# Kernel tuning notes

Hardware: AMD Instinct MI355X
Metric: run time of the kernel (lower is better)

The kernel has to match this reference:

```python
import jax, jax.numpy as jnp
import numpy as np

D, H, W = 128, 96, 96  # voxel grid
EPS = 1e-5

_OFFS = np.array([[dz, dy, dx] for dz in (-1, 0, 1) for dy in (-1, 0, 1) for dx in (-1, 0, 1)], dtype=np.int64)


def _flat(c):
    return (c[:, 0] * H + c[:, 1]) * W + c[:, 2]


def _dilate(coords):
    # union of coords + all 27 offsets, clipped to grid bounds (stride-1, pad-1 SparseConv3d output sites)
    p = coords[None, :, :] + _OFFS[:, None, :]          # [27, N, 3]
    p = p.reshape(-1, 3)
    ok = np.all((p >= 0) & (p < np.array([D, H, W])), axis=1)
    keys = np.unique(_flat(p[ok]))
    out = np.stack([keys // (H * W), (keys // W) % H, keys % W], axis=1)
    return out


def _rulebook(in_coords, out_coords):
    # nb[k, m] = row index into in_coords of (out_coords[m] + off_k), or -1
    lut = -np.ones(D * H * W, dtype=np.int32)
    lut[_flat(in_coords)] = np.arange(len(in_coords), dtype=np.int32)
    nb = np.full((27, len(out_coords)), -1, dtype=np.int32)
    for k, o in enumerate(_OFFS):
        p = out_coords + o
        ok = np.all((p >= 0) & (p < np.array([D, H, W])), axis=1)
        nb[k, ok] = lut[_flat(p[ok])]
    return nb


def setup_inputs() -> dict:
    key = jax.random.key(0)
    ks = jax.random.split(key, 20)
    # active sites: full plane z=64 over 96x96 footprint (surface-like sparse scene)
    yy, xx = np.meshgrid(np.arange(H), np.arange(W), indexing='ij')
    coords0 = np.stack([np.full(H * W, 64), yy.ravel(), xx.ravel()], axis=1).astype(np.int64)
    coords1 = _dilate(coords0)   # 27648 sites
    coords2 = _dilate(coords1)   # 46080 sites
    nb1 = jnp.asarray(_rulebook(coords0, coords1))
    nbs = jnp.asarray(_rulebook(coords1, coords1))
    nb2 = jnp.asarray(_rulebook(coords1, coords2))

    s = 0.05
    inp = {
        'x': jax.random.normal(ks[0], (coords0.shape[0], 256), jnp.float32),
        'w_s1': jax.random.normal(ks[1], (27, 256, 128), jnp.float32) * s,
        'g_s1': jax.random.uniform(ks[2], (128,), jnp.float32, 0.5, 1.5),
        'b_s1': jax.random.normal(ks[3], (128,), jnp.float32) * 0.1,
        'w11': jax.random.normal(ks[4], (27, 128, 128), jnp.float32) * s,
        'g11': jax.random.uniform(ks[5], (128,), jnp.float32, 0.5, 1.5),
        'b11': jax.random.normal(ks[6], (128,), jnp.float32) * 0.1,
        'w12': jax.random.normal(ks[7], (27, 128, 128), jnp.float32) * s,
        'g12': jax.random.uniform(ks[8], (128,), jnp.float32, 0.5, 1.5),
        'b12': jax.random.normal(ks[9], (128,), jnp.float32) * 0.1,
        'w21': jax.random.normal(ks[10], (27, 128, 128), jnp.float32) * s,
        'g21': jax.random.uniform(ks[11], (128,), jnp.float32, 0.5, 1.5),
        'b21': jax.random.normal(ks[12], (128,), jnp.float32) * 0.1,
        'w22': jax.random.normal(ks[13], (27, 128, 128), jnp.float32) * s,
        'g22': jax.random.uniform(ks[14], (128,), jnp.float32, 0.5, 1.5),
        'b22': jax.random.normal(ks[15], (128,), jnp.float32) * 0.1,
        'w_s2': jax.random.normal(ks[16], (27, 128, 32), jnp.float32) * s,
        'g_s2': jax.random.uniform(ks[17], (32,), jnp.float32, 0.5, 1.5),
        'b_s2': jax.random.normal(ks[18], (32,), jnp.float32) * 0.1,
        'nb1': nb1, 'nbs': nbs, 'nb2': nb2,
    }
    return inp


def _sparse_conv(x, nb, w):
    # gather -> GEMM -> accumulate per kernel offset (rulebook semantics of spconv)
    mask = nb >= 0                      # [27, M]
    idx = jnp.where(mask, nb, 0)
    out = jnp.zeros((nb.shape[1], w.shape[2]), x.dtype)
    for k in range(nb.shape[0]):        # fixed 27-offset loop
        g = jnp.where(mask[k][:, None], x[idx[k]], 0.0)  # [M, Cin]
        out = out + g @ w[k]
    return out


def _bn(f, g, b):
    # BatchNorm1d in training mode over active voxel rows (biased variance)
    mu = jnp.mean(f, axis=0)
    var = jnp.mean(jnp.square(f - mu), axis=0)
    return (f - mu) * jax.lax.rsqrt(var + EPS) * g + b


def _block(f, nbs, w1, g1, b1, w2, g2, b2):
    idn = f
    h = jax.nn.relu(_bn(_sparse_conv(f, nbs, w1), g1, b1))
    h = _bn(_sparse_conv(h, nbs, w2), g2, b2)
    return jax.nn.relu(h + idn)


def reference(x, w_s1, g_s1, b_s1, w11, g11, b11, w12, g12, b12,
              w21, g21, b21, w22, g22, b22, w_s2, g_s2, b_s2,
              nb1, nbs, nb2):
    f = jax.nn.relu(_bn(_sparse_conv(x, nb1, w_s1), g_s1, b_s1))          # spconv1
    f = _block(f, nbs, w11, g11, b11, w12, g12, b12)                      # block1 (submanifold)
    f = _block(f, nbs, w21, g21, b21, w22, g22, b22)                      # block2 (submanifold)
    out = jax.nn.relu(_bn(_sparse_conv(f, nb2, w_s2), g_s2, b_s2))        # spconv2
    return out  # features of the final SparseConvTensor, [46080, 32]
```

## Files before the change

kernel.cpp:

```cpp
#include <hip/hip_runtime.h>
#include <stdint.h>

typedef _Float16 f16;
typedef _Float16 f16x8 __attribute__((ext_vector_type(8)));
typedef _Float16 f16x4 __attribute__((ext_vector_type(4)));
typedef float f32x4 __attribute__((ext_vector_type(4)));

#define GAS __attribute__((address_space(1)))
#define LAS __attribute__((address_space(3)))

__device__ __forceinline__ void gl_lds16(const void* g, void* l) {
    __builtin_amdgcn_global_load_lds((const GAS uint32_t*)g, (LAS uint32_t*)l, 16, 0, 0);
}

__global__ __launch_bounds__(256) void zerof(float* __restrict__ p, int n) {
    int i = blockIdx.x * 256 + threadIdx.x;
    if (i < n) p[i] = 0.f;
}

__global__ __launch_bounds__(256) void cvt16(const float* __restrict__ in,
                                             f16* __restrict__ o, long n) {
    long i = (long)blockIdx.x * 256 + threadIdx.x;
    if (i < n) o[i] = (f16)in[i];
}

__global__ __launch_bounds__(256) void wtrans16(const float* __restrict__ w,
                                                f16* __restrict__ wt,
                                                int Cin, int Cout) {
    long i = (long)blockIdx.x * 256 + threadIdx.x;
    long total = 27L * Cin * Cout;
    if (i >= total) return;
    int ci = (int)(i % Cin);
    long t = i / Cin;
    int co = (int)(t % Cout);
    int k  = (int)(t / Cout);
    wt[i] = (f16)w[((long)k * Cin + ci) * Cout + co];
}

template <int LAYER>
__global__ __launch_bounds__(512, 2) void conv_dense(
    const f16* __restrict__ fin, const f16* __restrict__ wt,
    const f16* __restrict__ zrow, float* __restrict__ out,
    float* __restrict__ stats) {
    constexpr int COUT = (LAYER == 2) ? 32 : 128;
    constexpr int INRB = (LAYER == 0) ? 512 : 256;
    constexpr int WRB  = (LAYER == 0) ? 512 : 256;
    constexpr int RT   = (COUT == 128) ? 4 : 2;
    constexpr int CT   = (COUT == 128) ? 4 : 2;
    constexpr int NBCH = COUT / 4;
    extern __shared__ char smem[];
    char* ldsA0 = smem;
    char* ldsA1 = smem + 46080;
    char* ldsB0 = smem + 92160;
    char* ldsB1 = smem + 92160 + COUT * 256;

    const int b = blockIdx.x;
    const int p = b / 72;
    const int t0 = b % 72;
    const int y0 = (t0 / 6) * 8;
    const int x0 = (t0 % 6) * 16;
    const int tid = threadIdx.x;
    const int lane = tid & 63;
    const int wave = tid >> 6;
    const int kh = wave & 1;
    const int pairId = wave >> 1;
    const int q = lane >> 4;
    const int r16 = lane & 15;
    const int wr = ((COUT == 128) ? (pairId >> 1) : pairId) * (RT * 16);
    const int wc = ((COUT == 128) ? (pairId & 1) : 0) * (CT * 16);

    int S = 0;
    int js[3], dzs[3], hs[3];
    if (LAYER == 0) {
        js[0] = 0; dzs[0] = 1 - p; hs[0] = 0;
        js[1] = 0; dzs[1] = 1 - p; hs[1] = 1;
        S = 2;
    } else if (LAYER == 1) {
        for (int dz = -1; dz <= 1; dz++) {
            int j = p + dz;
            if (0 <= j && j < 3) { js[S] = j; dzs[S] = dz; hs[S] = 0; S++; }
        }
    } else {
        for (int dz = -1; dz <= 1; dz++) {
            int j = p + dz - 1;
            if (0 <= j && j < 3) { js[S] = j; dzs[S] = dz; hs[S] = 0; S++; }
        }
    }

    auto stageA = [&](int s, char* buf) {
        const int j = js[s], h = hs[s];
        const long pbase = (long)j * 9216;
        for (int ch = wave; ch < 45; ch += 8) {
            int site = ch * 4 + q;
            int sy = site / 18;
            int sx = site - sy * 18;
            int y = y0 - 1 + sy;
            int x = x0 - 1 + sx;
            int cc = r16 ^ (site & 7);
            bool ok = ((unsigned)y < 96u) & ((unsigned)x < 96u);
            const char* src = ok
                ? (const char*)fin + (pbase + y * 96 + x) * INRB + h * 256 + cc * 16
                : (const char*)zrow + cc * 16;
            gl_lds16(src, buf + ch * 1024);
        }
    };
    auto stageB = [&](int k, int h, char* buf) {
        for (int ch = wave; ch < NBCH; ch += 8) {
            int col = ch * 4 + q;
            int cc = r16 ^ (col & 7);
            const char* src = (const char*)wt + (long)(k * COUT + col) * WRB +
                              h * 256 + cc * 16;
            gl_lds16(src, buf + ch * 1024);
        }
    };

    f32x4 acc[RT][CT];
#pragma unroll
    for (int tr = 0; tr < RT; tr++)
#pragma unroll
        for (int c = 0; c < CT; c++) acc[tr][c] = f32x4{0.f, 0.f, 0.f, 0.f};

    stageA(0, ldsA0);
    stageB((dzs[0] + 1) * 9, hs[0], ldsB0);

    int tap = 0;
    for (int s = 0; s < S; s++) {
        const char* bufA = (s & 1) ? ldsA1 : ldsA0;
#pragma unroll
        for (int i = 0; i < 9; i++, tap++) {
            __syncthreads();
            if (i == 0 && s + 1 < S) stageA(s + 1, ((s + 1) & 1) ? ldsA1 : ldsA0);
            if (tap + 1 < S * 9) {
                int sn = (i == 8) ? s + 1 : s;
                int in2 = (i == 8) ? 0 : i + 1;
                stageB((dzs[sn] + 1) * 9 + in2, hs[sn], ((tap + 1) & 1) ? ldsB1 : ldsB0);
            }
            const char* bufB = (tap & 1) ? ldsB1 : ldsB0;
            const int dy = i / 3 - 1, dx = i % 3 - 1;
#pragma unroll
            for (int kk2 = 0; kk2 < 2; kk2++) {
                const int kk = kh * 2 + kk2;
                f16x8 Af[RT], Bf[CT];
#pragma unroll
                for (int tr = 0; tr < RT; tr++) {
                    int site = (wr / 16 + tr + 1 + dy) * 18 + 1 + dx + r16;
                    Af[tr] = *(const f16x8*)(bufA + site * 256 +
                                             (((kk * 4 + q) ^ (site & 7)) << 4));
                }
#pragma unroll
                for (int c = 0; c < CT; c++) {
                    int col = wc + c * 16 + r16;
                    Bf[c] = *(const f16x8*)(bufB + col * 256 +
                                            (((kk * 4 + q) ^ (col & 7)) << 4));
                }
#pragma unroll
                for (int tr = 0; tr < RT; tr++)
#pragma unroll
                    for (int c = 0; c < CT; c++)
                        acc[tr][c] = __builtin_amdgcn_mfma_f32_16x16x32_f16(
                            Af[tr], Bf[c], acc[tr][c], 0, 0, 0);
            }
        }
    }

    char* xch = smem + 92160;
    constexpr int XR = RT * CT * 1024;
    __syncthreads();
    if (kh == 1) {
#pragma unroll
        for (int tr = 0; tr < RT; tr++)
#pragma unroll
            for (int c = 0; c < CT; c++)
                *(f32x4*)(xch + pairId * XR + (tr * CT + c) * 1024 + lane * 16) =
                    acc[tr][c];
    }
    __syncthreads();
    if (kh == 1) return;
#pragma unroll
    for (int tr = 0; tr < RT; tr++)
#pragma unroll
        for (int c = 0; c < CT; c++)
            acc[tr][c] += *(const f32x4*)(xch + pairId * XR + (tr * CT + c) * 1024 +
                                          lane * 16);

    const long mbase = (long)p * 9216 + (long)y0 * 96 + x0;
#pragma unroll
    for (int c = 0; c < CT; c++) {
        const int col = wc + c * 16 + r16;
        float sum = 0.f, ssq = 0.f;
#pragma unroll
        for (int tr = 0; tr < RT; tr++) {
            const int ly = wr / 16 + tr;
#pragma unroll
            for (int r = 0; r < 4; r++) {
                const int lx = q * 4 + r;
                float v = acc[tr][c][r];
                out[(mbase + ly * 96 + lx) * COUT + col] = v;
                sum += v;
                ssq = fmaf(v, v, ssq);
            }
        }
        sum += __shfl_xor(sum, 16);
        sum += __shfl_xor(sum, 32);
        ssq += __shfl_xor(ssq, 16);
        ssq += __shfl_xor(ssq, 32);
        if (q == 0) {
            atomicAdd(&stats[col], sum);
            atomicAdd(&stats[COUT + col], ssq);
        }
    }
}

__global__ __launch_bounds__(256) void bn_apply4(
    const float4* __restrict__ f, const float* __restrict__ sums,
    const float* __restrict__ g, const float* __restrict__ bta,
    const f16x4* __restrict__ idn, f16* __restrict__ outh,
    float4* __restrict__ outf, long n4, int C, float invM) {
    long i = (long)blockIdx.x * 256 + threadIdx.x;
    if (i >= n4) return;
    int col0 = (int)((i * 4) & (C - 1));
    float4 v = f[i];
    float r[4] = {v.x, v.y, v.z, v.w};
    f16x4 id = {};
    if (idn) id = idn[i];
    f16x4 ho;
#pragma unroll
    for (int j = 0; j < 4; j++) {
        int c = col0 + j;
        float mu = sums[c] * invM;
        float var = sums[C + c] * invM - mu * mu;
        var = fmaxf(var, 0.f);
        float sc = g[c] * rsqrtf(var + 1e-5f);
        float x = (r[j] - mu) * sc + bta[c];
        if (idn) x += (float)id[j];
        x = fmaxf(x, 0.f);
        r[j] = x;
        ho[j] = (f16)x;
    }
    if (outf) outf[i] = make_float4(r[0], r[1], r[2], r[3]);
    else *(f16x4*)(outh + i * 4) = ho;
}

extern "C" void kernel_launch(void* const* d_in, const int* in_sizes, int n_in,
                              void* d_out, int out_size, void* d_ws, size_t ws_size,
                              hipStream_t stream) {
    (void)n_in; (void)out_size; (void)ws_size;
    const float* x    = (const float*)d_in[0];
    const float* w_s1 = (const float*)d_in[1];
    const float* g_s1 = (const float*)d_in[2];
    const float* b_s1 = (const float*)d_in[3];
    const float* w11  = (const float*)d_in[4];
    const float* g11  = (const float*)d_in[5];
    const float* b11  = (const float*)d_in[6];
    const float* w12  = (const float*)d_in[7];
    const float* g12  = (const float*)d_in[8];
    const float* b12  = (const float*)d_in[9];
    const float* w21  = (const float*)d_in[10];
    const float* g21  = (const float*)d_in[11];
    const float* b21  = (const float*)d_in[12];
    const float* w22  = (const float*)d_in[13];
    const float* g22  = (const float*)d_in[14];
    const float* b22  = (const float*)d_in[15];
    const float* w_s2 = (const float*)d_in[16];
    const float* g_s2 = (const float*)d_in[17];
    const float* b_s2 = (const float*)d_in[18];

    const int N0 = in_sizes[0] / 256;
    const int M1 = in_sizes[19] / 27;
    const int M2 = in_sizes[21] / 27;

    char* base = (char*)d_ws;
    size_t off = 0;
    auto alloc = [&](size_t bytes) -> char* {
        off = (off + 255) & ~(size_t)255;
        char* p = base + off;
        off += bytes;
        return p;
    };
    f16* xh  = (f16*)alloc((size_t)N0 * 256 * 2);
    f16* w1  = (f16*)alloc(27UL * 128 * 256 * 2);
    f16* wa1 = (f16*)alloc(27UL * 128 * 128 * 2);
    f16* wa2 = (f16*)alloc(27UL * 128 * 128 * 2);
    f16* wb1 = (f16*)alloc(27UL * 128 * 128 * 2);
    f16* wb2 = (f16*)alloc(27UL * 128 * 128 * 2);
    f16* w2  = (f16*)alloc(27UL * 32 * 128 * 2);
    f16* fA  = (f16*)alloc((size_t)M1 * 128 * 2);
    f16* fB  = (f16*)alloc((size_t)M1 * 128 * 2);
    float* cbuf  = (float*)alloc((size_t)M1 * 128 * 4);
    float* stats = (float*)alloc(1344UL * 4);
    f16*   zrow  = (f16*)alloc(512);

    const int lds01 = 92160 + 2 * 128 * 256;
    const int lds2  = 92160 + 2 * 32 * 256;
    (void)hipFuncSetAttribute((const void*)conv_dense<0>,
                              hipFuncAttributeMaxDynamicSharedMemorySize, lds01);
    (void)hipFuncSetAttribute((const void*)conv_dense<1>,
                              hipFuncAttributeMaxDynamicSharedMemorySize, lds01);
    (void)hipFuncSetAttribute((const void*)conv_dense<2>,
                              hipFuncAttributeMaxDynamicSharedMemorySize, lds2);

    zerof<<<6, 256, 0, stream>>>(stats, 1472);

    long nx = (long)N0 * 256;
    cvt16<<<(int)((nx + 255) / 256), 256, 0, stream>>>(x, xh, nx);
    wtrans16<<<(27 * 256 * 128 + 255) / 256, 256, 0, stream>>>(w_s1, w1, 256, 128);
    wtrans16<<<(27 * 128 * 128 + 255) / 256, 256, 0, stream>>>(w11, wa1, 128, 128);
    wtrans16<<<(27 * 128 * 128 + 255) / 256, 256, 0, stream>>>(w12, wa2, 128, 128);
    wtrans16<<<(27 * 128 * 128 + 255) / 256, 256, 0, stream>>>(w21, wb1, 128, 128);
    wtrans16<<<(27 * 128 * 128 + 255) / 256, 256, 0, stream>>>(w22, wb2, 128, 128);
    wtrans16<<<(27 * 128 * 32 + 255) / 256, 256, 0, stream>>>(w_s2, w2, 128, 32);

    const float inv1 = 1.f / (float)M1, inv2 = 1.f / (float)M2;
    const int g1 = 3 * 72;
    const int g2 = 5 * 72;
    const long n4a = (long)M1 * 128 / 4;
    const long n4b = (long)M2 * 32 / 4;
    const int ga = (int)((n4a + 255) / 256);
    const int gb = (int)((n4b + 255) / 256);

    conv_dense<0><<<g1, 512, lds01, stream>>>(xh, w1, zrow, cbuf, stats);
    bn_apply4<<<ga, 256, 0, stream>>>((float4*)cbuf, stats, g_s1, b_s1,
                                      nullptr, fA, nullptr, n4a, 128, inv1);
    conv_dense<1><<<g1, 512, lds01, stream>>>(fA, wa1, zrow, cbuf, stats + 256);
    bn_apply4<<<ga, 256, 0, stream>>>((float4*)cbuf, stats + 256, g11, b11,
                                      nullptr, fB, nullptr, n4a, 128, inv1);
    conv_dense<1><<<g1, 512, lds01, stream>>>(fB, wa2, zrow, cbuf, stats + 512);
    bn_apply4<<<ga, 256, 0, stream>>>((float4*)cbuf, stats + 512, g12, b12,
                                      (const f16x4*)fA, fA, nullptr, n4a, 128, inv1);
    conv_dense<1><<<g1, 512, lds01, stream>>>(fA, wb1, zrow, cbuf, stats + 768);
    bn_apply4<<<ga, 256, 0, stream>>>((float4*)cbuf, stats + 768, g21, b21,
                                      nullptr, fB, nullptr, n4a, 128, inv1);
    conv_dense<1><<<g1, 512, lds01, stream>>>(fB, wb2, zrow, cbuf, stats + 1024);
    bn_apply4<<<ga, 256, 0, stream>>>((float4*)cbuf, stats + 1024, g22, b22,
                                      (const f16x4*)fA, fA, nullptr, n4a, 128, inv1);
    conv_dense<2><<<g2, 512, lds2, stream>>>(fA, w2, zrow, cbuf, stats + 1280);
    bn_apply4<<<gb, 256, 0, stream>>>((float4*)cbuf, stats + 1280, g_s2, b_s2,
                                      nullptr, nullptr, (float4*)d_out, n4b, 32, inv2);
}
```

Baseline: 405.8 us.

## Split conv K dimension four ways across waves and reorder layer-2 blocks

Work is now split across the 8 waves as 2 row groups by 4 K-slices instead of 4 output tiles by 2 K-halves. Each wave covers the full output-channel width for its rows and a quarter of the channel depth, then partial sums are combined with a two-stage LDS reduction. For the 32-channel final layer, blocks are also remapped so the middle planes are scheduled first. The aim is more reuse of the A fragments across columns and fewer redundant LDS loads, at the cost of a larger reduction phase and more accumulator registers in the 128-channel layers.

```diff
diff --git a/kernel.cpp b/kernel.cpp
--- a/kernel.cpp
+++ b/kernel.cpp
@@ -45,8 +45,8 @@
     constexpr int COUT = (LAYER == 2) ? 32 : 128;
     constexpr int INRB = (LAYER == 0) ? 512 : 256;
     constexpr int WRB  = (LAYER == 0) ? 512 : 256;
-    constexpr int RT   = (COUT == 128) ? 4 : 2;
-    constexpr int CT   = (COUT == 128) ? 4 : 2;
+    constexpr int RT   = 4;
+    constexpr int CT   = COUT / 16;
     constexpr int NBCH = COUT / 4;
     extern __shared__ char smem[];
     char* ldsA0 = smem;
@@ -54,7 +54,11 @@
     char* ldsB0 = smem + 92160;
     char* ldsB1 = smem + 92160 + COUT * 256;
 
-    const int b = blockIdx.x;
+    int b = blockIdx.x;
+    if (LAYER == 2) {
+        const int order[5] = {2, 1, 3, 0, 4};
+        b = order[b / 72] * 72 + (b % 72);
+    }
     const int p = b / 72;
     const int t0 = b % 72;
     const int y0 = (t0 / 6) * 8;
@@ -62,12 +66,10 @@
     const int tid = threadIdx.x;
     const int lane = tid & 63;
     const int wave = tid >> 6;
-    const int kh = wave & 1;
-    const int pairId = wave >> 1;
+    const int kh = wave & 3;
+    const int rg = wave >> 2;
     const int q = lane >> 4;
     const int r16 = lane & 15;
-    const int wr = ((COUT == 128) ? (pairId >> 1) : pairId) * (RT * 16);
-    const int wc = ((COUT == 128) ? (pairId & 1) : 0) * (CT * 16);
 
     int S = 0;
     int js[3], dzs[3], hs[3];
@@ -137,60 +139,73 @@
             }
             const char* bufB = (tap & 1) ? ldsB1 : ldsB0;
             const int dy = i / 3 - 1, dx = i % 3 - 1;
-#pragma unroll
-            for (int kk2 = 0; kk2 < 2; kk2++) {
-                const int kk = kh * 2 + kk2;
-                f16x8 Af[RT], Bf[CT];
-#pragma unroll
-                for (int tr = 0; tr < RT; tr++) {
-                    int site = (wr / 16 + tr + 1 + dy) * 18 + 1 + dx + r16;
-                    Af[tr] = *(const f16x8*)(bufA + site * 256 +
-                                             (((kk * 4 + q) ^ (site & 7)) << 4));
-                }
-#pragma unroll
-                for (int c = 0; c < CT; c++) {
-                    int col = wc + c * 16 + r16;
-                    Bf[c] = *(const f16x8*)(bufB + col * 256 +
-                                            (((kk * 4 + q) ^ (col & 7)) << 4));
-                }
-#pragma unroll
-                for (int tr = 0; tr < RT; tr++)
-#pragma unroll
-                    for (int c = 0; c < CT; c++)
-                        acc[tr][c] = __builtin_amdgcn_mfma_f32_16x16x32_f16(
-                            Af[tr], Bf[c], acc[tr][c], 0, 0, 0);
+            f16x8 Af[RT], Bf[CT];
+#pragma unroll
+            for (int tr = 0; tr < RT; tr++) {
+                int site = (rg * 4 + tr + 1 + dy) * 18 + 1 + dx + r16;
+                Af[tr] = *(const f16x8*)(bufA + site * 256 +
+                                         (((kh * 4 + q) ^ (site & 7)) << 4));
             }
-        }
-    }
-
-    char* xch = smem + 92160;
+#pragma unroll
+            for (int c = 0; c < CT; c++) {
+                int col = c * 16 + r16;
+                Bf[c] = *(const f16x8*)(bufB + col * 256 +
+                                        (((kh * 4 + q) ^ (col & 7)) << 4));
+            }
+#pragma unroll
+            for (int tr = 0; tr < RT; tr++)
+#pragma unroll
+                for (int c = 0; c < CT; c++)
+                    acc[tr][c] = __builtin_amdgcn_mfma_f32_16x16x32_f16(
+                        Af[tr], Bf[c], acc[tr][c], 0, 0, 0);
+        }
+    }
+
     constexpr int XR = RT * CT * 1024;
+    char* xch = smem;
     __syncthreads();
+    if (kh >= 2) {
+#pragma unroll
+        for (int tr = 0; tr < RT; tr++)
+#pragma unroll
+            for (int c = 0; c < CT; c++)
+                *(f32x4*)(xch + (rg * 2 + (kh - 2)) * XR + (tr * CT + c) * 1024 +
+                          lane * 16) = acc[tr][c];
+    }
+    __syncthreads();
+    if (kh < 2) {
+#pragma unroll
+        for (int tr = 0; tr < RT; tr++)
+#pragma unroll
+            for (int c = 0; c < CT; c++)
+                acc[tr][c] += *(const f32x4*)(xch + (rg * 2 + kh) * XR +
+                                              (tr * CT + c) * 1024 + lane * 16);
+    }
     if (kh == 1) {
 #pragma unroll
         for (int tr = 0; tr < RT; tr++)
 #pragma unroll
             for (int c = 0; c < CT; c++)
-                *(f32x4*)(xch + pairId * XR + (tr * CT + c) * 1024 + lane * 16) =
-                    acc[tr][c];
+                *(f32x4*)(xch + (rg * 2 + 1) * XR + (tr * CT + c) * 1024 +
+                          lane * 16) = acc[tr][c];
     }
     __syncthreads();
-    if (kh == 1) return;
+    if (kh != 0) return;
 #pragma unroll
     for (int tr = 0; tr < RT; tr++)
 #pragma unroll
         for (int c = 0; c < CT; c++)
-            acc[tr][c] += *(const f32x4*)(xch + pairId * XR + (tr * CT + c) * 1024 +
-                                          lane * 16);
+            acc[tr][c] += *(const f32x4*)(xch + (rg * 2 + 1) * XR +
+                                          (tr * CT + c) * 1024 + lane * 16);
 
     const long mbase = (long)p * 9216 + (long)y0 * 96 + x0;
 #pragma unroll
     for (int c = 0; c < CT; c++) {
-        const int col = wc + c * 16 + r16;
+        const int col = c * 16 + r16;
         float sum = 0.f, ssq = 0.f;
 #pragma unroll
         for (int tr = 0; tr < RT; tr++) {
-            const int ly = wr / 16 + tr;
+            const int ly = rg * 4 + tr;
 #pragma unroll
             for (int r = 0; r < 4; r++) {
                 const int lx = q * 4 + r;
```

New measurement: 410.1 us. No clear change (+1.1%).

## Load conv weights directly into registers and drop per-tap LDS barriers

Applied to the files above, without the earlier changes.

Weight fragments are now loaded straight from global memory into registers and prefetched one tap ahead, so they no longer pass through double-buffered LDS. Only one barrier per plane stage remains instead of one per tap, and the LDS footprint shrinks to the input tile. The last layer's blocks are also reordered so that the central planes are scheduled first. In exchange each wave issues redundant global reads of the weights, which rely on L1/L2 hits, and register pressure rises from holding two sets of B fragments.

```diff
diff --git a/kernel.cpp b/kernel.cpp
--- a/kernel.cpp
+++ b/kernel.cpp
@@ -44,17 +44,18 @@
     float* __restrict__ stats) {
     constexpr int COUT = (LAYER == 2) ? 32 : 128;
     constexpr int INRB = (LAYER == 0) ? 512 : 256;
-    constexpr int WRB  = (LAYER == 0) ? 512 : 256;
+    constexpr int WRBe = (LAYER == 0) ? 256 : 128;
     constexpr int RT   = (COUT == 128) ? 4 : 2;
     constexpr int CT   = (COUT == 128) ? 4 : 2;
-    constexpr int NBCH = COUT / 4;
     extern __shared__ char smem[];
     char* ldsA0 = smem;
     char* ldsA1 = smem + 46080;
-    char* ldsB0 = smem + 92160;
-    char* ldsB1 = smem + 92160 + COUT * 256;
-
-    const int b = blockIdx.x;
+
+    int b = blockIdx.x;
+    if (LAYER == 2) {
+        const int order[5] = {2, 1, 3, 0, 4};
+        b = order[b / 72] * 72 + (b % 72);
+    }
     const int p = b / 72;
     const int t0 = b % 72;
     const int y0 = (t0 / 6) * 8;
@@ -104,14 +105,16 @@
             gl_lds16(src, buf + ch * 1024);
         }
     };
-    auto stageB = [&](int k, int h, char* buf) {
-        for (int ch = wave; ch < NBCH; ch += 8) {
-            int col = ch * 4 + q;
-            int cc = r16 ^ (col & 7);
-            const char* src = (const char*)wt + (long)(k * COUT + col) * WRB +
-                              h * 256 + cc * 16;
-            gl_lds16(src, buf + ch * 1024);
-        }
+
+    auto loadB = [&](int ktap, int h, f16x8 (&B)[2][CT]) {
+#pragma unroll
+        for (int kk2 = 0; kk2 < 2; kk2++)
+#pragma unroll
+            for (int c = 0; c < CT; c++) {
+                int col = wc + c * 16 + r16;
+                B[kk2][c] = *(const f16x8*)(wt + (long)(ktap * COUT + col) * WRBe +
+                                            h * 128 + ((kh * 2 + kk2) * 4 + q) * 8);
+            }
     };
 
     f32x4 acc[RT][CT];
@@ -121,26 +124,27 @@
         for (int c = 0; c < CT; c++) acc[tr][c] = f32x4{0.f, 0.f, 0.f, 0.f};
 
     stageA(0, ldsA0);
-    stageB((dzs[0] + 1) * 9, hs[0], ldsB0);
+    f16x8 Bc[2][CT], Bn[2][CT];
+    loadB((dzs[0] + 1) * 9, hs[0], Bc);
 
     int tap = 0;
+    const int T = S * 9;
     for (int s = 0; s < S; s++) {
         const char* bufA = (s & 1) ? ldsA1 : ldsA0;
+        __syncthreads();
+        if (s + 1 < S) stageA(s + 1, ((s + 1) & 1) ? ldsA1 : ldsA0);
 #pragma unroll
         for (int i = 0; i < 9; i++, tap++) {
-            __syncthreads();
-            if (i == 0 && s + 1 < S) stageA(s + 1, ((s + 1) & 1) ? ldsA1 : ldsA0);
-            if (tap + 1 < S * 9) {
+            if (tap + 1 < T) {
                 int sn = (i == 8) ? s + 1 : s;
                 int in2 = (i == 8) ? 0 : i + 1;
-                stageB((dzs[sn] + 1) * 9 + in2, hs[sn], ((tap + 1) & 1) ? ldsB1 : ldsB0);
+                loadB((dzs[sn] + 1) * 9 + in2, hs[sn], Bn);
             }
-            const char* bufB = (tap & 1) ? ldsB1 : ldsB0;
             const int dy = i / 3 - 1, dx = i % 3 - 1;
 #pragma unroll
             for (int kk2 = 0; kk2 < 2; kk2++) {
                 const int kk = kh * 2 + kk2;
-                f16x8 Af[RT], Bf[CT];
+                f16x8 Af[RT];
 #pragma unroll
                 for (int tr = 0; tr < RT; tr++) {
                     int site = (wr / 16 + tr + 1 + dy) * 18 + 1 + dx + r16;
@@ -148,22 +152,20 @@
                                              (((kk * 4 + q) ^ (site & 7)) << 4));
                 }
 #pragma unroll
-                for (int c = 0; c < CT; c++) {
-                    int col = wc + c * 16 + r16;
-                    Bf[c] = *(const f16x8*)(bufB + col * 256 +
-                                            (((kk * 4 + q) ^ (col & 7)) << 4));
-                }
-#pragma unroll
                 for (int tr = 0; tr < RT; tr++)
 #pragma unroll
                     for (int c = 0; c < CT; c++)
                         acc[tr][c] = __builtin_amdgcn_mfma_f32_16x16x32_f16(
-                            Af[tr], Bf[c], acc[tr][c], 0, 0, 0);
+                            Af[tr], Bc[kk2][c], acc[tr][c], 0, 0, 0);
             }
-        }
-    }
-
-    char* xch = smem + 92160;
+#pragma unroll
+            for (int kk2 = 0; kk2 < 2; kk2++)
+#pragma unroll
+                for (int c = 0; c < CT; c++) Bc[kk2][c] = Bn[kk2][c];
+        }
+    }
+
+    char* xch = smem;
     constexpr int XR = RT * CT * 1024;
     __syncthreads();
     if (kh == 1) {
@@ -290,14 +292,13 @@
     float* stats = (float*)alloc(1344UL * 4);
     f16*   zrow  = (f16*)alloc(512);
 
-    const int lds01 = 92160 + 2 * 128 * 256;
-    const int lds2  = 92160 + 2 * 32 * 256;
+    const int ldsAB = 92160;
     (void)hipFuncSetAttribute((const void*)conv_dense<0>,
-                              hipFuncAttributeMaxDynamicSharedMemorySize, lds01);
+                              hipFuncAttributeMaxDynamicSharedMemorySize, ldsAB);
     (void)hipFuncSetAttribute((const void*)conv_dense<1>,
-                              hipFuncAttributeMaxDynamicSharedMemorySize, lds01);
+                              hipFuncAttributeMaxDynamicSharedMemorySize, ldsAB);
     (void)hipFuncSetAttribute((const void*)conv_dense<2>,
-                              hipFuncAttributeMaxDynamicSharedMemorySize, lds2);
+                              hipFuncAttributeMaxDynamicSharedMemorySize, ldsAB);
 
     zerof<<<6, 256, 0, stream>>>(stats, 1472);
 
@@ -318,22 +319,22 @@
     const int ga = (int)((n4a + 255) / 256);
     const int gb = (int)((n4b + 255) / 256);
 
-    conv_dense<0><<<g1, 512, lds01, stream>>>(xh, w1, zrow, cbuf, stats);
+    conv_dense<0><<<g1, 512, ldsAB, stream>>>(xh, w1, zrow, cbuf, stats);
     bn_apply4<<<ga, 256, 0, stream>>>((float4*)cbuf, stats, g_s1, b_s1,
                                       nullptr, fA, nullptr, n4a, 128, inv1);
-    conv_dense<1><<<g1, 512, lds01, stream>>>(fA, wa1, zrow, cbuf, stats + 256);
+    conv_dense<1><<<g1, 512, ldsAB, stream>>>(fA, wa1, zrow, cbuf, stats + 256);
     bn_apply4<<<ga, 256, 0, stream>>>((float4*)cbuf, stats + 256, g11, b11,
                                       nullptr, fB, nullptr, n4a, 128, inv1);
-    conv_dense<1><<<g1, 512, lds01, stream>>>(fB, wa2, zrow, cbuf, stats + 512);
+    conv_dense<1><<<g1, 512, ldsAB, stream>>>(fB, wa2, zrow, cbuf, stats + 512);
     bn_apply4<<<ga, 256, 0, stream>>>((float4*)cbuf, stats + 512, g12, b12,
                                       (const f16x4*)fA, fA, nullptr, n4a, 128, inv1);
-    conv_dense<1><<<g1, 512, lds01, stream>>>(fA, wb1, zrow, cbuf, stats + 768);
+    conv_dense<1><<<g1, 512, ldsAB, stream>>>(fA, wb1, zrow, cbuf, stats + 768);
     bn_apply4<<<ga, 256, 0, stream>>>((float4*)cbuf, stats + 768, g21, b21,
                                       nullptr, fB, nullptr, n4a, 128, inv1);
-    conv_dense<1><<<g1, 512, lds01, stream>>>(fB, wb2, zrow, cbuf, stats + 1024);
+    conv_dense<1><<<g1, 512, ldsAB, stream>>>(fB, wb2, zrow, cbuf, stats + 1024);
     bn_apply4<<<ga, 256, 0, stream>>>((float4*)cbuf, stats + 1024, g22, b22,
                                       (const f16x4*)fA, fA, nullptr, n4a, 128, inv1);
-    conv_dense<2><<<g2, 512, lds2, stream>>>(fA, w2, zrow, cbuf, stats + 1280);
+    conv_dense<2><<<g2, 512, ldsAB, stream>>>(fA, w2, zrow, cbuf, stats + 1280);
     bn_apply4<<<gb, 256, 0, stream>>>((float4*)cbuf, stats + 1280, g_s2, b_s2,
                                       nullptr, nullptr, (float4*)d_out, n4b, 32, inv2);
 }
```

Result: slower. 601.4 us (+48.2%).

## Triple-buffer weight panels with vmcnt waits, single-buffer input tile, reorder layer-2 blocks

Applied to the files above, without the earlier changes.

The input tile drops from double to single buffering, and the weight panels go from double to triple buffering with a prefetch distance of two taps. Each tap now waits with an explicit s_waitcnt vmcnt plus a raw s_barrier instead of a full __syncthreads, so weight loads can stay in flight across taps. This cuts LDS use per block (better occupancy at 2 blocks/CU) and overlaps weight fetches more deeply. In exchange, each plane switch now stalls on two full barriers while the input tile reloads. Layer 2 also remaps block order so the heavier middle planes start first.

```diff
diff --git a/kernel.cpp b/kernel.cpp
--- a/kernel.cpp
+++ b/kernel.cpp
@@ -48,13 +48,17 @@
     constexpr int RT   = (COUT == 128) ? 4 : 2;
     constexpr int CT   = (COUT == 128) ? 4 : 2;
     constexpr int NBCH = COUT / 4;
+    constexpr int BLN  = (COUT == 128) ? 4 : 1;
+    constexpr int BPAN = COUT * 256;
     extern __shared__ char smem[];
-    char* ldsA0 = smem;
-    char* ldsA1 = smem + 46080;
-    char* ldsB0 = smem + 92160;
-    char* ldsB1 = smem + 92160 + COUT * 256;
-
-    const int b = blockIdx.x;
+    char* ldsA = smem;
+    char* ldsB = smem + 46080;
+
+    int b = blockIdx.x;
+    if (LAYER == 2) {
+        const int order[5] = {2, 1, 3, 0, 4};
+        b = order[b / 72] * 72 + (b % 72);
+    }
     const int p = b / 72;
     const int t0 = b % 72;
     const int y0 = (t0 / 6) * 8;
@@ -87,7 +91,7 @@
         }
     }
 
-    auto stageA = [&](int s, char* buf) {
+    auto stageA = [&](int s) {
         const int j = js[s], h = hs[s];
         const long pbase = (long)j * 9216;
         for (int ch = wave; ch < 45; ch += 8) {
@@ -101,10 +105,14 @@
             const char* src = ok
                 ? (const char*)fin + (pbase + y * 96 + x) * INRB + h * 256 + cc * 16
                 : (const char*)zrow + cc * 16;
-            gl_lds16(src, buf + ch * 1024);
+            gl_lds16(src, ldsA + ch * 1024);
         }
     };
-    auto stageB = [&](int k, int h, char* buf) {
+    auto stageB = [&](int t) {
+        const int sn = t / 9, in2 = t % 9;
+        const int k = (dzs[sn] + 1) * 9 + in2;
+        const int h = hs[sn];
+        char* buf = ldsB + (t % 3) * BPAN;
         for (int ch = wave; ch < NBCH; ch += 8) {
             int col = ch * 4 + q;
             int cc = r16 ^ (col & 7);
@@ -120,22 +128,31 @@
 #pragma unroll
         for (int c = 0; c < CT; c++) acc[tr][c] = f32x4{0.f, 0.f, 0.f, 0.f};
 
-    stageA(0, ldsA0);
-    stageB((dzs[0] + 1) * 9, hs[0], ldsB0);
+    const int T = S * 9;
+    stageA(0);
+    stageB(0);
+    stageB(1);
 
     int tap = 0;
     for (int s = 0; s < S; s++) {
-        const char* bufA = (s & 1) ? ldsA1 : ldsA0;
+        if (s > 0) {
+            __syncthreads();
+            stageA(s);
+            __syncthreads();
+        }
 #pragma unroll
         for (int i = 0; i < 9; i++, tap++) {
-            __syncthreads();
-            if (i == 0 && s + 1 < S) stageA(s + 1, ((s + 1) & 1) ? ldsA1 : ldsA0);
-            if (tap + 1 < S * 9) {
-                int sn = (i == 8) ? s + 1 : s;
-                int in2 = (i == 8) ? 0 : i + 1;
-                stageB((dzs[sn] + 1) * 9 + in2, hs[sn], ((tap + 1) & 1) ? ldsB1 : ldsB0);
+            if (tap == T - 1) {
+                asm volatile("s_waitcnt vmcnt(0)" ::: "memory");
+            } else if constexpr (BLN == 4) {
+                asm volatile("s_waitcnt vmcnt(4)" ::: "memory");
+            } else {
+                asm volatile("s_waitcnt vmcnt(1)" ::: "memory");
             }
-            const char* bufB = (tap & 1) ? ldsB1 : ldsB0;
+            __builtin_amdgcn_s_barrier();
+            asm volatile("" ::: "memory");
+            if (tap + 2 < T) stageB(tap + 2);
+            const char* bufB = ldsB + (tap % 3) * BPAN;
             const int dy = i / 3 - 1, dx = i % 3 - 1;
 #pragma unroll
             for (int kk2 = 0; kk2 < 2; kk2++) {
@@ -144,7 +161,7 @@
 #pragma unroll
                 for (int tr = 0; tr < RT; tr++) {
                     int site = (wr / 16 + tr + 1 + dy) * 18 + 1 + dx + r16;
-                    Af[tr] = *(const f16x8*)(bufA + site * 256 +
+                    Af[tr] = *(const f16x8*)(ldsA + site * 256 +
                                              (((kk * 4 + q) ^ (site & 7)) << 4));
                 }
 #pragma unroll
@@ -163,7 +180,7 @@
         }
     }
 
-    char* xch = smem + 92160;
+    char* xch = smem;
     constexpr int XR = RT * CT * 1024;
     __syncthreads();
     if (kh == 1) {
@@ -290,8 +307,8 @@
     float* stats = (float*)alloc(1344UL * 4);
     f16*   zrow  = (f16*)alloc(512);
 
-    const int lds01 = 92160 + 2 * 128 * 256;
-    const int lds2  = 92160 + 2 * 32 * 256;
+    const int lds01 = 46080 + 3 * 128 * 256;
+    const int lds2  = 46080 + 3 * 32 * 256;
     (void)hipFuncSetAttribute((const void*)conv_dense<0>,
                               hipFuncAttributeMaxDynamicSharedMemorySize, lds01);
     (void)hipFuncSetAttribute((const void*)conv_dense<1>,
```

New measurement: 424.2 us. 4.5% more time.
